# Kernel tuning notes

Measured on AMD Instinct MI355X. Metric: run time of the kernel, lower is better.

## Reference

```python
import jax, jax.numpy as jnp
import numpy as np

B, S, D = 4, 2048, 2048
H, KVH = 16, 4
HD = D // H            # 128
N_REP = H // KVH       # 4
SCALE = HD ** -0.5


def setup_inputs() -> dict:
    key = jax.random.key(0)
    ks = jax.random.split(key, 10)
    w = 0.02
    x = jax.random.normal(ks[0], (B, S, D), jnp.float32)
    # Linear weights stored as [in, out] (y = x @ W + b, equivalent to torch Linear)
    Wq = jax.random.normal(ks[1], (D, D), jnp.float32) * w
    bq = jnp.zeros((D,), jnp.float32)
    Wk = jax.random.normal(ks[2], (D, KVH * HD), jnp.float32) * w
    bk = jnp.zeros((KVH * HD,), jnp.float32)
    Wv = jax.random.normal(ks[3], (D, KVH * HD), jnp.float32) * w
    bv = jnp.zeros((KVH * HD,), jnp.float32)
    Wo = jax.random.normal(ks[4], (D, D), jnp.float32) * w
    bo = jnp.zeros((D,), jnp.float32)
    # RoPE tables: freqs_cis is [max_seq_len, head_dim//2] complex -> cos/sin
    inv_freq = 1.0 / (10000.0 ** (jnp.arange(0, HD, 2, dtype=jnp.float32) / HD))  # [HD//2]
    t = jnp.arange(S, dtype=jnp.float32)
    ang = jnp.outer(t, inv_freq)                     # [S, HD//2]
    freqs_cos = jnp.cos(ang)
    freqs_sin = jnp.sin(ang)
    # causal additive mask [1,1,S,S]
    neg = jnp.float32(-1e9)
    mask = jnp.where(jnp.triu(jnp.ones((S, S), bool), k=1), neg, 0.0)[None, None]
    return {"x": x, "Wq": Wq, "bq": bq, "Wk": Wk, "bk": bk, "Wv": Wv, "bv": bv,
            "Wo": Wo, "bo": bo, "freqs_cos": freqs_cos, "freqs_sin": freqs_sin,
            "mask": mask, "start_pos": 0}


def _apply_rope(q, k, cos, sin):
    # q: [B,S,H,HD], k: [B,S,KVH,HD]; interleaved complex pairs on last dim
    def rot(t):
        tr = t.reshape(*t.shape[:-1], HD // 2, 2)
        xr, xi = tr[..., 0], tr[..., 1]
        c = cos[None, :, None, :]
        s = sin[None, :, None, :]
        yr = xr * c - xi * s
        yi = xr * s + xi * c
        return jnp.stack([yr, yi], axis=-1).reshape(t.shape)
    return rot(q), rot(k)


def reference(x, Wq, bq, Wk, bk, Wv, bv, Wo, bo, freqs_cos, freqs_sin, mask, start_pos):
    Bx, Sx, _ = x.shape
    q = (x @ Wq + bq).reshape(Bx, Sx, H, HD)
    k = (x @ Wk + bk).reshape(Bx, Sx, KVH, HD)
    v = (x @ Wv + bv).reshape(Bx, Sx, KVH, HD)
    q, k = _apply_rope(q, k, freqs_cos, freqs_sin)
    # start_pos = 0 prefill: cache write-then-read is identity, so use k, v directly
    q = q.transpose(0, 2, 1, 3)                      # [B,H,S,HD]
    k = k.transpose(0, 2, 1, 3)                      # [B,KVH,S,HD]
    v = v.transpose(0, 2, 1, 3)
    k = jnp.repeat(k, N_REP, axis=1)                 # repeat_kv -> [B,H,S,HD]
    v = jnp.repeat(v, N_REP, axis=1)
    scores = jnp.einsum("bhsd,bhtd->bhst", q, k) * SCALE + mask
    w = jax.nn.softmax(scores, axis=-1)              # dropout p=0 -> identity
    out = jnp.einsum("bhst,bhtd->bhsd", w, v)
    out = out.transpose(0, 2, 1, 3).reshape(Bx, Sx, D)
    return out @ Wo + bo
```

## Files before the change

### kernel.cpp

```cpp
#include <hip/hip_runtime.h>

typedef unsigned short u16t;
typedef __bf16 bf16x8 __attribute__((ext_vector_type(8)));
typedef float f32x4 __attribute__((ext_vector_type(4)));
typedef unsigned short ushort4_t __attribute__((ext_vector_type(4)));
typedef unsigned short ushort8_t __attribute__((ext_vector_type(8)));

#define B_    4
#define S_    2048
#define D_    2048
#define H_    16
#define KVH_  4
#define HD_   128
#define KDIM  2048
#define SCALE_ 0.08838834764831845f

__device__ __forceinline__ u16t f2bf(float f){
    unsigned u; __builtin_memcpy(&u, &f, 4);
    u += 0x7fffu + ((u >> 16) & 1u);
    return (u16t)(u >> 16);
}
__device__ __forceinline__ void glds16(const u16t* g, u16t* l){
    __builtin_amdgcn_global_load_lds((const __attribute__((address_space(1))) void*)g,
                                     (__attribute__((address_space(3))) void*)l, 16, 0, 0);
}
__device__ __forceinline__ void wg_barrier_lgkm(){
    __builtin_amdgcn_sched_barrier(0);
    asm volatile("s_waitcnt lgkmcnt(0)" ::: "memory");
    __builtin_amdgcn_s_barrier();
    __builtin_amdgcn_sched_barrier(0);
}

__global__ void f32_to_bf16(const float* __restrict__ in, u16t* __restrict__ out)
{
    int i = (blockIdx.x * 256 + threadIdx.x) * 4;
    float4 v = *(const float4*)(in + i);
    ushort4_t p;
    p[0] = f2bf(v.x); p[1] = f2bf(v.y); p[2] = f2bf(v.z); p[3] = f2bf(v.w);
    *(ushort4_t*)(out + i) = p;
}

__global__ void transpose_f32_bf16(const float* __restrict__ W, u16t* __restrict__ Wt,
                                   int Ncols, int Krows)
{
    __shared__ u16t tile[32][33];
    int tx = threadIdx.x, ty = threadIdx.y;
    int n = blockIdx.x * 32 + tx, k = blockIdx.y * 32 + ty;
    tile[ty][tx] = f2bf(W[(size_t)k * Ncols + n]);
    __syncthreads();
    int nn = blockIdx.x * 32 + ty, kk = blockIdx.y * 32 + tx;
    Wt[(size_t)nn * Krows + kk] = tile[tx][ty];
}

#define GEMM_PROLOGUE_AND_KLOOP                                                   \
    __shared__ u16t As[128 * 32];                                                 \
    __shared__ u16t Bs[128 * 32];                                                 \
    const int tid  = threadIdx.x;                                                 \
    const int lane = tid & 63, w = tid >> 6;                                      \
    const int wr = (w >> 1) * 64, wc = (w & 1) * 64;                              \
    const int lr = lane & 15, quad = lane >> 4;                                   \
    const int m0 = blockIdx.y * 128, n0 = blockIdx.x * 128;                       \
    f32x4 acc[4][4];                                                              \
    _Pragma("unroll")                                                             \
    for (int r = 0; r < 4; r++)                                                   \
        _Pragma("unroll")                                                         \
        for (int c = 0; c < 4; c++) acc[r][c] = (f32x4){0.f, 0.f, 0.f, 0.f};      \
    for (int k0 = 0; k0 < KDIM; k0 += 32) {                                       \
        __syncthreads();                                                          \
        _Pragma("unroll")                                                         \
        for (int cc = 0; cc < 2; cc++) {                                          \
            int slot = tid + cc * 256;                                            \
            int row = slot >> 2, ko = (slot & 3) * 8;                             \
            glds16(A  + (size_t)(m0 + row) * KDIM + k0 + ko, As + slot * 8);      \
            glds16(Bt + (size_t)(n0 + row) * KDIM + k0 + ko, Bs + slot * 8);      \
        }                                                                         \
        __syncthreads();                                                          \
        bf16x8 a[4], b[4];                                                        \
        _Pragma("unroll")                                                         \
        for (int r = 0; r < 4; r++)                                               \
            a[r] = *(const bf16x8*)(As + (wr + r * 16 + lr) * 32 + quad * 8);     \
        _Pragma("unroll")                                                         \
        for (int c = 0; c < 4; c++)                                               \
            b[c] = *(const bf16x8*)(Bs + (wc + c * 16 + lr) * 32 + quad * 8);     \
        _Pragma("unroll")                                                         \
        for (int r = 0; r < 4; r++)                                               \
            _Pragma("unroll")                                                     \
            for (int c = 0; c < 4; c++)                                           \
                acc[r][c] = __builtin_amdgcn_mfma_f32_16x16x32_bf16(a[r], b[c], acc[r][c], 0, 0, 0); \
    }

__global__ void gemm_o(const u16t* __restrict__ A, const u16t* __restrict__ Bt,
                       const float* __restrict__ bias, float* __restrict__ out)
{
    GEMM_PROLOGUE_AND_KLOOP
#pragma unroll
    for (int r = 0; r < 4; r++) {
#pragma unroll
        for (int c = 0; c < 4; c++) {
            int n = n0 + wc + c * 16 + lr;
            float bval = bias[n];
#pragma unroll
            for (int g = 0; g < 4; g++) {
                int m = m0 + wr + r * 16 + quad * 4 + g;
                out[(size_t)m * D_ + n] = acc[r][c][g] + bval;
            }
        }
    }
}

__global__ void gemm_qkv(const u16t* __restrict__ A, const u16t* __restrict__ Bt,
                         const float* __restrict__ bq, const float* __restrict__ bk,
                         const float* __restrict__ bv,
                         u16t* __restrict__ q_t, u16t* __restrict__ k_t,
                         u16t* __restrict__ v_t,
                         const float* __restrict__ fc, const float* __restrict__ fs)
{
    GEMM_PROLOGUE_AND_KLOOP
    const int region = (blockIdx.x < 16) ? 0 : ((blockIdx.x < 20) ? 1 : 2);
#pragma unroll
    for (int r = 0; r < 4; r++) {
#pragma unroll
        for (int c = 0; c < 4; c++) {
            int n = n0 + wc + c * 16 + lr;
            if (region == 0) {
                float bval = bq[n];
                int hh = n >> 7, d = n & 127, i2 = d >> 1;
#pragma unroll
                for (int g = 0; g < 4; g++) {
                    int m = m0 + wr + r * 16 + quad * 4 + g;
                    int bb = m >> 11, s = m & (S_ - 1);
                    float v = acc[r][c][g] + bval;
                    float p = __shfl_xor(v, 1);
                    float cf = fc[s * 64 + i2], sf = fs[s * 64 + i2];
                    float o = (d & 1) ? (p * sf + v * cf) : (v * cf - p * sf);
                    q_t[(((size_t)bb * H_ + hh) * S_ + s) * HD_ + d] = f2bf(o);
                }
            } else if (region == 1) {
                int nk = n - 2048;
                float bval = bk[nk];
                int hh = nk >> 7, d = nk & 127, i2 = d >> 1;
#pragma unroll
                for (int g = 0; g < 4; g++) {
                    int m = m0 + wr + r * 16 + quad * 4 + g;
                    int bb = m >> 11, s = m & (S_ - 1);
                    float v = acc[r][c][g] + bval;
                    float p = __shfl_xor(v, 1);
                    float cf = fc[s * 64 + i2], sf = fs[s * 64 + i2];
                    float o = (d & 1) ? (p * sf + v * cf) : (v * cf - p * sf);
                    k_t[(((size_t)bb * KVH_ + hh) * S_ + s) * HD_ + d] = f2bf(o);
                }
            } else {
                int nv = n - 2560;
                float bval = bv[nv];
                int kv = nv >> 7, d = nv & 127;
                int mb = m0 + wr + r * 16 + quad * 4;
                int bb = mb >> 11, s = mb & (S_ - 1);
                ushort4_t pk;
#pragma unroll
                for (int g = 0; g < 4; g++) pk[g] = f2bf(acc[r][c][g] + bval);
                *(ushort4_t*)(v_t + (((size_t)bb * KVH_ + kv) * HD_ + d) * S_ + s) = pk;
            }
        }
    }
}

#define KSTRIDE 136
#define VSTRIDE 40
__global__ __launch_bounds__(512) void
attn_kernel(const u16t* __restrict__ qt, const u16t* __restrict__ kt,
            const u16t* __restrict__ vt, u16t* __restrict__ att)
{
    __shared__ u16t Ks[2][32 * KSTRIDE];
    __shared__ u16t Vs[2][128 * VSTRIDE];
    __shared__ u16t Ps[128 * VSTRIDE];
    const int tid  = threadIdx.x;
    const int lane = tid & 63, w = tid >> 6;
    const int lr = lane & 15, quad = lane >> 4;
    const int bh = blockIdx.y, b = bh >> 4, h = bh & 15, kv = h >> 2;
    const int q0 = ((int)gridDim.x - 1 - (int)blockIdx.x) * 128;

    const u16t* qb = qt + (((size_t)b * H_ + h) * S_ + q0) * HD_;
    const u16t* kb = kt + ((size_t)b * KVH_ + kv) * S_ * HD_;
    const u16t* vb = vt + ((size_t)b * KVH_ + kv) * HD_ * S_;

    bf16x8 qa[4];
#pragma unroll
    for (int ks = 0; ks < 4; ks++)
        qa[ks] = *(const bf16x8*)(qb + (w * 16 + lr) * HD_ + ks * 32 + quad * 8);

    f32x4 o[8];
#pragma unroll
    for (int i = 0; i < 8; i++) o[i] = (f32x4){0.f, 0.f, 0.f, 0.f};
    float lpart[4] = {0.f, 0.f, 0.f, 0.f};

    const int krow = tid >> 4, kgi = tid & 15;
    const int vrow = tid >> 2, vgi = tid & 3;

    const int ntile = q0 / 32 + 4;
    ushort8_t kr[2], vr[2];
#pragma unroll
    for (int p = 0; p < 2; p++) {
        kr[p] = *(const ushort8_t*)(kb + (size_t)(p * 32 + krow) * HD_ + kgi * 8);
        vr[p] = *(const ushort8_t*)(vb + (size_t)vrow * S_ + p * 32 + vgi * 8);
    }

    for (int it = 0; it < ntile; it += 2) {
#pragma unroll
        for (int p = 0; p < 2; p++) {
            const int t0 = (it + p) * 32;
            *(ushort8_t*)(&Ks[p][krow * KSTRIDE + kgi * 8]) = kr[p];
            *(ushort8_t*)(&Vs[p][vrow * VSTRIDE + vgi * 8]) = vr[p];
            const int tn0 = (it + p + 2 < ntile) ? (it + p + 2) * 32 : 0;
            kr[p] = *(const ushort8_t*)(kb + (size_t)(tn0 + krow) * HD_ + kgi * 8);
            vr[p] = *(const ushort8_t*)(vb + (size_t)vrow * S_ + tn0 + vgi * 8);
            wg_barrier_lgkm();

            f32x4 sc[2];
            sc[0] = (f32x4){0.f, 0.f, 0.f, 0.f};
            sc[1] = (f32x4){0.f, 0.f, 0.f, 0.f};
            __builtin_amdgcn_s_setprio(1);
#pragma unroll
            for (int tn = 0; tn < 2; tn++)
#pragma unroll
                for (int ks = 0; ks < 4; ks++) {
                    bf16x8 kf = *(const bf16x8*)(&Ks[p][(tn * 16 + lr) * KSTRIDE + ks * 32 + quad * 8]);
                    sc[tn] = __builtin_amdgcn_mfma_f32_16x16x32_bf16(qa[ks], kf, sc[tn], 0, 0, 0);
                }
            __builtin_amdgcn_s_setprio(0);

            if (t0 + 31 <= q0 + w * 16) {
#pragma unroll
                for (int g = 0; g < 4; g++)
#pragma unroll
                    for (int tn = 0; tn < 2; tn++)
                        sc[tn][g] = __expf(sc[tn][g] * SCALE_);
            } else {
#pragma unroll
                for (int g = 0; g < 4; g++) {
                    int srow = q0 + w * 16 + quad * 4 + g;
#pragma unroll
                    for (int tn = 0; tn < 2; tn++) {
                        int tc = t0 + tn * 16 + lr;
                        sc[tn][g] = __expf(sc[tn][g] * SCALE_ + ((tc > srow) ? -1e9f : 0.f));
                    }
                }
            }
#pragma unroll
            for (int g = 0; g < 4; g++) {
                lpart[g] += sc[0][g] + sc[1][g];
#pragma unroll
                for (int tn = 0; tn < 2; tn++)
                    Ps[(w * 16 + quad * 4 + g) * VSTRIDE + tn * 16 + lr] = f2bf(sc[tn][g]);
            }
            bf16x8 pa = *(const bf16x8*)(Ps + (w * 16 + lr) * VSTRIDE + quad * 8);
            __builtin_amdgcn_s_setprio(1);
#pragma unroll
            for (int nt = 0; nt < 8; nt++) {
                bf16x8 vf = *(const bf16x8*)(&Vs[p][(nt * 16 + lr) * VSTRIDE + quad * 8]);
                o[nt] = __builtin_amdgcn_mfma_f32_16x16x32_bf16(pa, vf, o[nt], 0, 0, 0);
            }
            __builtin_amdgcn_s_setprio(0);
        }
    }

#pragma unroll
    for (int g = 0; g < 4; g++) {
        float l = lpart[g];
        l += __shfl_xor(l, 1);
        l += __shfl_xor(l, 2);
        l += __shfl_xor(l, 4);
        l += __shfl_xor(l, 8);
        float inv = 1.f / l;
        int s = q0 + w * 16 + quad * 4 + g;
#pragma unroll
        for (int nt = 0; nt < 8; nt++) {
            int d = nt * 16 + lr;
            att[((size_t)(b * S_ + s)) * D_ + h * HD_ + d] = f2bf(o[nt][g] * inv);
        }
    }
}

extern "C" void kernel_launch(void* const* d_in, const int* in_sizes, int n_in,
                              void* d_out, int out_size, void* d_ws, size_t ws_size,
                              hipStream_t stream)
{
    const float* x  = (const float*)d_in[0];
    const float* Wq = (const float*)d_in[1];
    const float* bq = (const float*)d_in[2];
    const float* Wk = (const float*)d_in[3];
    const float* bk = (const float*)d_in[4];
    const float* Wv = (const float*)d_in[5];
    const float* bv = (const float*)d_in[6];
    const float* Wo = (const float*)d_in[7];
    const float* bo = (const float*)d_in[8];
    const float* fc = (const float*)d_in[9];
    const float* fs = (const float*)d_in[10];

    const size_t M1 = (size_t)1024 * 1024;
    u16t* ws   = (u16t*)d_ws;
    u16t* x_bf = ws;
    u16t* att  = ws;
    u16t* Wqt  = ws + 16 * M1;
    u16t* Wot  = ws + 16 * M1;
    u16t* Wkt  = ws + 20 * M1;
    u16t* Wvt  = ws + 21 * M1;
    u16t* k_t  = ws + 22 * M1;
    u16t* v_t  = ws + 26 * M1;
    u16t* q_t  = (u16t*)d_out;

    f32_to_bf16<<<dim3(16384), 256, 0, stream>>>(x, x_bf);

    dim3 tb(32, 32);
    transpose_f32_bf16<<<dim3(64, 64), tb, 0, stream>>>(Wq, Wqt, 2048, 2048);
    transpose_f32_bf16<<<dim3(16, 64), tb, 0, stream>>>(Wk, Wkt, 512, 2048);
    transpose_f32_bf16<<<dim3(16, 64), tb, 0, stream>>>(Wv, Wvt, 512, 2048);

    gemm_qkv<<<dim3(24, 64), 256, 0, stream>>>(x_bf, Wqt, bq, bk, bv,
                                               q_t, k_t, v_t, fc, fs);

    attn_kernel<<<dim3(16, 64), 512, 0, stream>>>(q_t, k_t, v_t, att);

    transpose_f32_bf16<<<dim3(64, 64), tb, 0, stream>>>(Wo, Wot, 2048, 2048);

    gemm_o<<<dim3(16, 64), 256, 0, stream>>>(att, Wot, bo, (float*)d_out);
}
```

Baseline: 578.3 us.

## Rewrite attention with 32x32x16 MFMA, register-resident P, and swizzled LDS

The attention kernel moves from 16x16x32 MFMA with 8 waves of 16 query rows to 32x32x16 MFMA with 4 waves of 32 rows, computing S^T so that P can stay in registers. P is packed with v_cvt_pk_bf16 and rearranged with permlane32_swap, which removes the LDS round-trip through Ps. K and V tiles use XOR-swizzled LDS layouts in place of padding, and waves skip fully masked key tiles after the barrier. The rewrite cuts LDS traffic and instruction count, but it relies on gfx950-specific instructions and an intricate lane mapping.

Measured after the change: 541.1 us. 6.4% less time.

```diff
diff --git a/kernel.cpp b/kernel.cpp
--- a/kernel.cpp
+++ b/kernel.cpp
@@ -3,6 +3,7 @@
 typedef unsigned short u16t;
 typedef __bf16 bf16x8 __attribute__((ext_vector_type(8)));
 typedef float f32x4 __attribute__((ext_vector_type(4)));
+typedef float f32x16 __attribute__((ext_vector_type(16)));
 typedef unsigned short ushort4_t __attribute__((ext_vector_type(4)));
 typedef unsigned short ushort8_t __attribute__((ext_vector_type(8)));
 
@@ -29,6 +30,14 @@
     asm volatile("s_waitcnt lgkmcnt(0)" ::: "memory");
     __builtin_amdgcn_s_barrier();
     __builtin_amdgcn_sched_barrier(0);
+}
+__device__ __forceinline__ unsigned cvt_pk_bf16(float lo, float hi){
+    unsigned r;
+    asm("v_cvt_pk_bf16_f32 %0, %1, %2" : "=v"(r) : "v"(lo), "v"(hi));
+    return r;
+}
+__device__ __forceinline__ void permlane32_swap(unsigned &a, unsigned &b){
+    asm volatile("v_permlane32_swap_b32 %0, %1" : "+v"(a), "+v"(b));
 }
 
 __global__ void f32_to_bf16(const float* __restrict__ in, u16t* __restrict__ out)
@@ -164,18 +173,15 @@
     }
 }
 
-#define KSTRIDE 136
-#define VSTRIDE 40
-__global__ __launch_bounds__(512) void
+__global__ __launch_bounds__(256, 2) void
 attn_kernel(const u16t* __restrict__ qt, const u16t* __restrict__ kt,
             const u16t* __restrict__ vt, u16t* __restrict__ att)
 {
-    __shared__ u16t Ks[2][32 * KSTRIDE];
-    __shared__ u16t Vs[2][128 * VSTRIDE];
-    __shared__ u16t Ps[128 * VSTRIDE];
+    __shared__ char Ks[2][8192];
+    __shared__ char Vs[2][8192];
     const int tid  = threadIdx.x;
     const int lane = tid & 63, w = tid >> 6;
-    const int lr = lane & 15, quad = lane >> 4;
+    const int l5 = lane & 31, hi = lane >> 5;
     const int bh = blockIdx.y, b = bh >> 4, h = bh & 15, kv = h >> 2;
     const int q0 = ((int)gridDim.x - 1 - (int)blockIdx.x) * 128;
 
@@ -183,100 +189,122 @@
     const u16t* kb = kt + ((size_t)b * KVH_ + kv) * S_ * HD_;
     const u16t* vb = vt + ((size_t)b * KVH_ + kv) * HD_ * S_;
 
-    bf16x8 qa[4];
-#pragma unroll
-    for (int ks = 0; ks < 4; ks++)
-        qa[ks] = *(const bf16x8*)(qb + (w * 16 + lr) * HD_ + ks * 32 + quad * 8);
-
-    f32x4 o[8];
-#pragma unroll
-    for (int i = 0; i < 8; i++) o[i] = (f32x4){0.f, 0.f, 0.f, 0.f};
-    float lpart[4] = {0.f, 0.f, 0.f, 0.f};
-
-    const int krow = tid >> 4, kgi = tid & 15;
-    const int vrow = tid >> 2, vgi = tid & 3;
+    bf16x8 qa[8];
+#pragma unroll
+    for (int ks = 0; ks < 8; ks++)
+        qa[ks] = *(const bf16x8*)(qb + (w * 32 + l5) * HD_ + ks * 16 + hi * 8);
+
+    f32x16 zero16;
+#pragma unroll
+    for (int j = 0; j < 16; j++) zero16[j] = 0.f;
+    f32x16 o[4];
+#pragma unroll
+    for (int i = 0; i < 4; i++) o[i] = zero16;
+    float lpart = 0.f;
+
+    const int krow = tid >> 4, kcol = tid & 15;
+    const int vd   = tid >> 2, vcol = tid & 3;
+    const int kw0 = ((krow     ) * 256 + kcol * 16) ^ ((krow & 7) << 4);
+    const int kw1 = ((krow + 16) * 256 + kcol * 16) ^ ((krow & 7) << 4);
+    const int vw0 = ((vd      ) * 64 + vcol * 16) ^ (((vd >> 1) & 3) << 5);
+    const int vw1 = ((vd + 64 ) * 64 + vcol * 16) ^ (((vd >> 1) & 3) << 5);
 
     const int ntile = q0 / 32 + 4;
-    ushort8_t kr[2], vr[2];
+    ushort8_t kr[2][2], vr[2][2];
 #pragma unroll
     for (int p = 0; p < 2; p++) {
-        kr[p] = *(const ushort8_t*)(kb + (size_t)(p * 32 + krow) * HD_ + kgi * 8);
-        vr[p] = *(const ushort8_t*)(vb + (size_t)vrow * S_ + p * 32 + vgi * 8);
+        int t0 = p * 32;
+        kr[p][0] = *(const ushort8_t*)(kb + (size_t)(t0 + krow     ) * HD_ + kcol * 8);
+        kr[p][1] = *(const ushort8_t*)(kb + (size_t)(t0 + krow + 16) * HD_ + kcol * 8);
+        vr[p][0] = *(const ushort8_t*)(vb + (size_t)(vd     ) * S_ + t0 + vcol * 8);
+        vr[p][1] = *(const ushort8_t*)(vb + (size_t)(vd + 64) * S_ + t0 + vcol * 8);
     }
 
     for (int it = 0; it < ntile; it += 2) {
 #pragma unroll
         for (int p = 0; p < 2; p++) {
             const int t0 = (it + p) * 32;
-            *(ushort8_t*)(&Ks[p][krow * KSTRIDE + kgi * 8]) = kr[p];
-            *(ushort8_t*)(&Vs[p][vrow * VSTRIDE + vgi * 8]) = vr[p];
+            *(ushort8_t*)(Ks[p] + kw0) = kr[p][0];
+            *(ushort8_t*)(Ks[p] + kw1) = kr[p][1];
+            *(ushort8_t*)(Vs[p] + vw0) = vr[p][0];
+            *(ushort8_t*)(Vs[p] + vw1) = vr[p][1];
             const int tn0 = (it + p + 2 < ntile) ? (it + p + 2) * 32 : 0;
-            kr[p] = *(const ushort8_t*)(kb + (size_t)(tn0 + krow) * HD_ + kgi * 8);
-            vr[p] = *(const ushort8_t*)(vb + (size_t)vrow * S_ + tn0 + vgi * 8);
+            kr[p][0] = *(const ushort8_t*)(kb + (size_t)(tn0 + krow     ) * HD_ + kcol * 8);
+            kr[p][1] = *(const ushort8_t*)(kb + (size_t)(tn0 + krow + 16) * HD_ + kcol * 8);
+            vr[p][0] = *(const ushort8_t*)(vb + (size_t)(vd     ) * S_ + tn0 + vcol * 8);
+            vr[p][1] = *(const ushort8_t*)(vb + (size_t)(vd + 64) * S_ + tn0 + vcol * 8);
             wg_barrier_lgkm();
 
-            f32x4 sc[2];
-            sc[0] = (f32x4){0.f, 0.f, 0.f, 0.f};
-            sc[1] = (f32x4){0.f, 0.f, 0.f, 0.f};
+            if (t0 > q0 + w * 32 + 31) continue;
+
+            f32x16 sa = zero16, sb = zero16;
             __builtin_amdgcn_s_setprio(1);
 #pragma unroll
-            for (int tn = 0; tn < 2; tn++)
-#pragma unroll
-                for (int ks = 0; ks < 4; ks++) {
-                    bf16x8 kf = *(const bf16x8*)(&Ks[p][(tn * 16 + lr) * KSTRIDE + ks * 32 + quad * 8]);
-                    sc[tn] = __builtin_amdgcn_mfma_f32_16x16x32_bf16(qa[ks], kf, sc[tn], 0, 0, 0);
+            for (int ks = 0; ks < 8; ks += 2) {
+                bf16x8 kf0 = *(const bf16x8*)(Ks[p] +
+                    ((l5 * 256 + ks * 32 + hi * 16) ^ ((l5 & 7) << 4)));
+                sa = __builtin_amdgcn_mfma_f32_32x32x16_bf16(kf0, qa[ks], sa, 0, 0, 0);
+                bf16x8 kf1 = *(const bf16x8*)(Ks[p] +
+                    ((l5 * 256 + (ks + 1) * 32 + hi * 16) ^ ((l5 & 7) << 4)));
+                sb = __builtin_amdgcn_mfma_f32_32x32x16_bf16(kf1, qa[ks + 1], sb, 0, 0, 0);
+            }
+            __builtin_amdgcn_s_setprio(0);
+            f32x16 sc = sa + sb;
+
+            float pr[16];
+            if (t0 + 31 <= q0 + w * 32) {
+#pragma unroll
+                for (int r = 0; r < 16; r++) pr[r] = __expf(sc[r] * SCALE_);
+            } else {
+                const int srow = q0 + w * 32 + l5;
+#pragma unroll
+                for (int r = 0; r < 16; r++) {
+                    int tc = t0 + (r & 3) + 8 * (r >> 2) + 4 * hi;
+                    pr[r] = __expf(sc[r] * SCALE_ + ((tc > srow) ? -1e9f : 0.f));
                 }
-            __builtin_amdgcn_s_setprio(0);
-
-            if (t0 + 31 <= q0 + w * 16) {
-#pragma unroll
-                for (int g = 0; g < 4; g++)
-#pragma unroll
-                    for (int tn = 0; tn < 2; tn++)
-                        sc[tn][g] = __expf(sc[tn][g] * SCALE_);
-            } else {
-#pragma unroll
-                for (int g = 0; g < 4; g++) {
-                    int srow = q0 + w * 16 + quad * 4 + g;
-#pragma unroll
-                    for (int tn = 0; tn < 2; tn++) {
-                        int tc = t0 + tn * 16 + lr;
-                        sc[tn][g] = __expf(sc[tn][g] * SCALE_ + ((tc > srow) ? -1e9f : 0.f));
-                    }
-                }
-            }
-#pragma unroll
-            for (int g = 0; g < 4; g++) {
-                lpart[g] += sc[0][g] + sc[1][g];
-#pragma unroll
-                for (int tn = 0; tn < 2; tn++)
-                    Ps[(w * 16 + quad * 4 + g) * VSTRIDE + tn * 16 + lr] = f2bf(sc[tn][g]);
-            }
-            bf16x8 pa = *(const bf16x8*)(Ps + (w * 16 + lr) * VSTRIDE + quad * 8);
+            }
+#pragma unroll
+            for (int r = 0; r < 16; r++) lpart += pr[r];
+
+            unsigned d0[4], d1[4];
+#pragma unroll
+            for (int q4 = 0; q4 < 4; q4++) {
+                d0[q4] = cvt_pk_bf16(pr[4 * q4 + 0], pr[4 * q4 + 1]);
+                d1[q4] = cvt_pk_bf16(pr[4 * q4 + 2], pr[4 * q4 + 3]);
+            }
+            permlane32_swap(d0[0], d0[1]);
+            permlane32_swap(d1[0], d1[1]);
+            permlane32_swap(d0[2], d0[3]);
+            permlane32_swap(d1[2], d1[3]);
+            union { unsigned u[4]; bf16x8 v; } pa0, pa1;
+            pa0.u[0] = d0[0]; pa0.u[1] = d1[0]; pa0.u[2] = d0[1]; pa0.u[3] = d1[1];
+            pa1.u[0] = d0[2]; pa1.u[1] = d1[2]; pa1.u[2] = d0[3]; pa1.u[3] = d1[3];
+
             __builtin_amdgcn_s_setprio(1);
 #pragma unroll
-            for (int nt = 0; nt < 8; nt++) {
-                bf16x8 vf = *(const bf16x8*)(&Vs[p][(nt * 16 + lr) * VSTRIDE + quad * 8]);
-                o[nt] = __builtin_amdgcn_mfma_f32_16x16x32_bf16(pa, vf, o[nt], 0, 0, 0);
+            for (int dt = 0; dt < 4; dt++) {
+                bf16x8 vf0 = *(const bf16x8*)(Vs[p] +
+                    (((dt * 32 + l5) * 64 + hi * 16) ^ (((l5 >> 1) & 3) << 5)));
+                o[dt] = __builtin_amdgcn_mfma_f32_32x32x16_bf16(pa0.v, vf0, o[dt], 0, 0, 0);
+                bf16x8 vf1 = *(const bf16x8*)(Vs[p] +
+                    (((dt * 32 + l5) * 64 + 32 + hi * 16) ^ (((l5 >> 1) & 3) << 5)));
+                o[dt] = __builtin_amdgcn_mfma_f32_32x32x16_bf16(pa1.v, vf1, o[dt], 0, 0, 0);
             }
             __builtin_amdgcn_s_setprio(0);
         }
     }
 
-#pragma unroll
-    for (int g = 0; g < 4; g++) {
-        float l = lpart[g];
-        l += __shfl_xor(l, 1);
-        l += __shfl_xor(l, 2);
-        l += __shfl_xor(l, 4);
-        l += __shfl_xor(l, 8);
-        float inv = 1.f / l;
-        int s = q0 + w * 16 + quad * 4 + g;
-#pragma unroll
-        for (int nt = 0; nt < 8; nt++) {
-            int d = nt * 16 + lr;
-            att[((size_t)(b * S_ + s)) * D_ + h * HD_ + d] = f2bf(o[nt][g] * inv);
-        }
+    float lf = lpart + __shfl_xor(lpart, 32);
+    float linv = 1.f / lf;
+#pragma unroll
+    for (int r = 0; r < 16; r++) {
+        int qrow = (r & 3) + 8 * (r >> 2) + 4 * hi;
+        float iv = __shfl(linv, qrow);
+        int s = q0 + w * 32 + qrow;
+        u16t* orow = att + ((size_t)(b * S_ + s)) * D_ + h * HD_ + l5;
+#pragma unroll
+        for (int dt = 0; dt < 4; dt++)
+            orow[dt * 32] = f2bf(o[dt][r] * iv);
     }
 }
 
@@ -318,7 +346,7 @@
     gemm_qkv<<<dim3(24, 64), 256, 0, stream>>>(x_bf, Wqt, bq, bk, bv,
                                                q_t, k_t, v_t, fc, fs);
 
-    attn_kernel<<<dim3(16, 64), 512, 0, stream>>>(q_t, k_t, v_t, att);
+    attn_kernel<<<dim3(16, 64), 256, 0, stream>>>(q_t, k_t, v_t, att);
 
     transpose_f32_bf16<<<dim3(64, 64), tb, 0, stream>>>(Wo, Wot, 2048, 2048);
 
```
